# Performance work log

Hardware: AMD Instinct MI355X
Metric: run time of the kernel (lower is better)

The kernel has to match this reference:

```python
import jax, jax.numpy as jnp
import numpy as np

N = 100000
E = 1600000
BN_EPS = 1e-5


def setup_inputs() -> dict:
    key = jax.random.key(0)
    ks = jax.random.split(key, 32)
    rn = lambda k, shape, s=0.05: jax.random.normal(k, shape, jnp.float32) * s
    inp = {
        "x": jax.random.normal(ks[0], (N, 2), jnp.float32),
        "edge_index": jax.random.randint(ks[1], (2, E), 0, N, dtype=jnp.int64),
        # GIN conv1 mlp: Linear(1,256) -> BN(256) -> ReLU -> Linear(256,128)
        "w1": rn(ks[2], (1, 256)), "b1": rn(ks[3], (256,)),
        "g1": jax.random.uniform(ks[4], (256,), jnp.float32, 0.5, 1.5),
        "be1": rn(ks[5], (256,)),
        "m1": rn(ks[6], (256,)),
        "v1": jax.random.uniform(ks[7], (256,), jnp.float32, 0.5, 1.5),
        "w2": rn(ks[8], (256, 128)), "b2": rn(ks[9], (128,)),
        # GIN conv2 mlp: Linear(128,64) -> BN(64) -> ReLU -> Linear(64,64)
        "w3": rn(ks[10], (128, 64)), "b3": rn(ks[11], (64,)),
        "g2": jax.random.uniform(ks[12], (64,), jnp.float32, 0.5, 1.5),
        "be2": rn(ks[13], (64,)),
        "m2": rn(ks[14], (64,)),
        "v2": jax.random.uniform(ks[15], (64,), jnp.float32, 0.5, 1.5),
        # Bilinear(64, 64, 96)
        "wb": rn(ks[16], (96, 64, 64)), "bb": rn(ks[17], (96,)),
        # linear3: 96 -> 6
        "w5": rn(ks[18], (96, 6)), "b5": rn(ks[19], (6,)),
        # linear2: 6 -> 6
        "w6": rn(ks[20], (6, 6)), "b6": rn(ks[21], (6,)),
    }
    return inp


def reference(x, edge_index, w1, b1, g1, be1, m1, v1, w2, b2,
              w3, b3, g2, be2, m2, v2, w4_unused=None, wb=None, bb=None,
              w5=None, b5=None, w6=None, b6=None):
    # note: kept signature explicit below; see _reference
    raise NotImplementedError


def _bn(h, g, b, m, v):
    # inference-mode batchnorm with running stats
    return (h - m) * jax.lax.rsqrt(v + BN_EPS) * g + b


def reference(x, edge_index, w1, b1, g1, be1, m1, v1, w2, b2,
              w3, b3, g2, be2, m2, v2, wb, bb, w5, b5, w6, b6):
    src, dst = edge_index[0], edge_index[1]
    n = x.shape[0]

    def agg(h):
        # GIN sum aggregation: (1+eps)*x + sum_{j in N(i)} x_j, eps=0
        return h + jax.ops.segment_sum(h[src], dst, num_segments=n)

    def block(col):  # col: [n, 1]
        h = agg(col)
        h = jnp.maximum(_bn(h @ w1 + b1, g1, be1, m1, v1), 0.0) @ w2 + b2  # [n,128]
        h = agg(h)
        h = jnp.maximum(_bn(h @ w3 + b3, g2, be2, m2, v2), 0.0)            # mlp2 ends with BN+ReLU? no:
        return h

    # mlp2 = Linear(128,64)->BN(64)->ReLU->Linear(64,64); rebuild correctly inline:
    def block2(col):
        h = agg(col)
        h = jnp.maximum(_bn(h @ w1 + b1, g1, be1, m1, v1), 0.0) @ w2 + b2  # [n,128]
        h = agg(h)
        h = jnp.maximum(_bn(h @ w3 + b3, g2, be2, m2, v2), 0.0)
        return h

    h1 = block2(x[:, 1:2])  # column tmp-1 = 1 first
    h2 = block2(x[:, 0:1])  # then column 0
    # mlp2's final Linear(64,64) is folded below? No -- apply final linear of mlp2:
    # (handled in block2 already via w3 only; second linear uses separate weights)
    hb = jnp.einsum('ni,kij,nj->nk', h1, wb, h2) + bb  # Bilinear(64,64,96)
    h = jnp.maximum(hb @ w5 + b5, 0.0)                 # relu(linear3)
    h = h @ w6 + b6                                    # linear2
    return jax.nn.log_softmax(h, axis=1)
```

## Files before the change

kernel.cpp:

```cpp
#include <hip/hip_runtime.h>
#include <hip/hip_bf16.h>

#define NN 100000
#define NE 1600000
#define EPS 1e-5f
#define NCHUNK 98
#define NB 196
#define BCAP2 10240
#define RND 8192
#define NRND 196

typedef __attribute__((ext_vector_type(8))) short short8;
typedef __attribute__((ext_vector_type(4))) float f32x4;

__device__ __forceinline__ float b2f_lo(unsigned u){ return __uint_as_float(u << 16); }
__device__ __forceinline__ float b2f_hi(unsigned u){ return __uint_as_float(u & 0xffff0000u); }
__device__ __forceinline__ float b2f_u(unsigned short u){ return __uint_as_float(((unsigned)u) << 16); }
__device__ __forceinline__ unsigned short f2b(float f){
  __hip_bfloat16 h = __float2bfloat16(f);
  return __builtin_bit_cast(unsigned short, h);
}

__global__ void k_probe(const int* __restrict__ ei32, int* __restrict__ flag, int* __restrict__ gcur){
  __shared__ int cnt;
  if (threadIdx.x == 0) cnt = 0;
  __syncthreads();
  if (ei32[threadIdx.x * 2 + 1] == 0) atomicAdd(&cnt, 1);
  __syncthreads();
  if (threadIdx.x == 0) flag[0] = (cnt > 200) ? 1 : 0;
  for (int i = threadIdx.x; i < NB; i += 256) gcur[i] = i * BCAP2;
}

__global__ __launch_bounds__(1024) void k_bin(const void* __restrict__ ei, const int* __restrict__ flag,
                                              int* __restrict__ gcur, int* __restrict__ staged){
  __shared__ int hcnt[256];
  __shared__ int pref[256];
  __shared__ int bnd[200];
  __shared__ int hrun[196];
  __shared__ int gb[196];
  __shared__ int sbuf[RND];
  int t = threadIdx.x;
  int base = blockIdx.x * RND;
  bool f64 = (flag[0] != 0);
  int pay[8], bkt[8];
  #pragma unroll
  for (int k = 0; k < 8; ++k){
    int e = base + k * 1024 + t;
    if (e < NE){
      int src, dst;
      if (f64){ src = (int)((const long long*)ei)[e]; dst = (int)((const long long*)ei)[NE + e]; }
      else    { src = ((const int*)ei)[e];            dst = ((const int*)ei)[NE + e]; }
      pay[k] = (src << 9) | (dst & 511);
      bkt[k] = dst >> 9;
    } else { pay[k] = 0; bkt[k] = -1; }
  }
  if (t < 256) hcnt[t] = 0;
  __syncthreads();
  #pragma unroll
  for (int k = 0; k < 8; ++k)
    if (bkt[k] >= 0) atomicAdd(&hcnt[bkt[k]], 1);
  __syncthreads();
  if (t < 256) pref[t] = hcnt[t];
  __syncthreads();
  for (int off = 1; off < 256; off <<= 1){
    int v = 0;
    if (t < 256 && t >= off) v = pref[t - off];
    __syncthreads();
    if (t < 256) pref[t] += v;
    __syncthreads();
  }
  if (t < 196){
    int excl = pref[t] - hcnt[t];
    bnd[t] = excl;
    hrun[t] = excl;
    gb[t] = (hcnt[t] > 0) ? atomicAdd(&gcur[t], hcnt[t]) : 0;
  }
  if (t == 196) bnd[196] = 0;
  __syncthreads();
  if (t == 0) bnd[196] = pref[255];
  __syncthreads();
  #pragma unroll
  for (int k = 0; k < 8; ++k)
    if (bkt[k] >= 0){
      int lp = atomicAdd(&hrun[bkt[k]], 1);
      sbuf[lp] = pay[k];
    }
  __syncthreads();
  int total = bnd[196];
  for (int i = t; i < total; i += 1024){
    int b = 0;
    #pragma unroll
    for (int sh = 128; sh > 0; sh >>= 1)
      if (b + sh <= 196 && bnd[b + sh] <= i) b += sh;
    staged[gb[b] + (i - bnd[b])] = sbuf[i];
  }
}

__global__ __launch_bounds__(256) void k_bdeg(const int* __restrict__ staged, const int* __restrict__ gcur,
                                              int* __restrict__ deg){
  __shared__ int dcnt[512];
  int b = blockIdx.x, t = threadIdx.x;
  for (int l = t; l < 512; l += 256) dcnt[l] = 0;
  __syncthreads();
  int cnt = min(gcur[b] - b * BCAP2, BCAP2);
  const int* sp = staged + b * BCAP2;
  for (int i = t; i < cnt; i += 256)
    atomicAdd(&dcnt[sp[i] & 511], 1);
  __syncthreads();
  for (int l = t; l < 512; l += 256){
    int n = b * 512 + l;
    if (n < NN) deg[n] = dcnt[l];
  }
}

__global__ void k_scan1(const int* __restrict__ deg, int* __restrict__ cinc, int* __restrict__ part){
  __shared__ int b[1024];
  int i = blockIdx.x * 1024 + threadIdx.x;
  int v = (i < NN) ? deg[i] : 0;
  b[threadIdx.x] = v; __syncthreads();
  for (int off = 1; off < 1024; off <<= 1){
    int t = (threadIdx.x >= off) ? b[threadIdx.x - off] : 0;
    __syncthreads();
    b[threadIdx.x] += t;
    __syncthreads();
  }
  if (i < NN) cinc[i] = b[threadIdx.x];
  if (threadIdx.x == 1023) part[blockIdx.x] = b[1023];
}

__global__ void k_scan2(int* __restrict__ part, int nchunk){
  __shared__ int b[128];
  int tid = threadIdx.x;
  int v = (tid < nchunk) ? part[tid] : 0;
  b[tid] = v; __syncthreads();
  for (int off = 1; off < 128; off <<= 1){
    int t = (tid >= off) ? b[tid - off] : 0;
    __syncthreads();
    b[tid] += t;
    __syncthreads();
  }
  if (tid < nchunk) part[tid] = b[tid] - v;
}

__global__ void k_scan3(const int* __restrict__ deg, const int* __restrict__ cinc,
                        const int* __restrict__ part, int* __restrict__ rowp){
  int i = blockIdx.x * 1024 + threadIdx.x;
  if (i < NN){
    rowp[i] = cinc[i] - deg[i] + part[blockIdx.x];
  }
  if (i == 0) rowp[NN] = NE;
}

__global__ __launch_bounds__(256) void k_scatter2(const int* __restrict__ staged, const int* __restrict__ gcur,
                                                  const int* __restrict__ rowp, int* __restrict__ colidx){
  __shared__ int cur[512];
  int b = blockIdx.x, t = threadIdx.x;
  for (int l = t; l < 512; l += 256){
    int n = b * 512 + l;
    cur[l] = (n < NN) ? rowp[n] : 0;
  }
  __syncthreads();
  int cnt = min(gcur[b] - b * BCAP2, BCAP2);
  const int* sp = staged + b * BCAP2;
  for (int i = t; i < cnt; i += 256){
    int p = sp[i];
    int pos = atomicAdd(&cur[p & 511], 1);
    colidx[pos] = p >> 9;
  }
}

__global__ void k_prep_sort(const float* __restrict__ w1, const float* __restrict__ b1,
                            const float* __restrict__ g1, const float* __restrict__ be1,
                            const float* __restrict__ m1, const float* __restrict__ v1,
                            const float* __restrict__ w3, const float* __restrict__ b3,
                            const float* __restrict__ g2, const float* __restrict__ be2,
                            const float* __restrict__ m2, const float* __restrict__ v2,
                            float* __restrict__ aC, float* __restrict__ cC,
                            float* __restrict__ thrS, int* __restrict__ pos,
                            unsigned short* __restrict__ w3s, float* __restrict__ b3p){
  __shared__ float key[256];
  __shared__ int idx[256];
  int tid = threadIdx.x;
  {
    float inv = rsqrtf(v1[tid] + EPS);
    float sc = g1[tid] * inv;
    float a = w1[tid] * sc;
    float c = (b1[tid] - m1[tid]) * sc + be1[tid];
    aC[tid] = a; cC[tid] = c;
    key[tid] = (a != 0.0f) ? (-c / a) : __int_as_float(0x7f800000);
    idx[tid] = tid;
  }
  __syncthreads();
  for (int k = 2; k <= 256; k <<= 1){
    for (int j = k >> 1; j > 0; j >>= 1){
      int ixj = tid ^ j;
      if (ixj > tid){
        float k1 = key[tid], k2 = key[ixj];
        bool asc = ((tid & k) == 0);
        if ((k1 > k2) == asc){
          int i1 = idx[tid];
          key[tid] = k2; key[ixj] = k1;
          idx[tid] = idx[ixj]; idx[ixj] = i1;
        }
      }
      __syncthreads();
    }
  }
  thrS[tid] = key[tid];
  pos[idx[tid]] = tid;
  if (tid < 64){
    float i2 = rsqrtf(v2[tid] + EPS);
    b3p[tid] = (b3[tid] - m2[tid]) * i2 * g2[tid] + be2[tid];
  }
  for (int id = tid; id < 8192; id += 256){
    int cs = id >> 11, r = id & 2047;
    int kt = r >> 9;  r &= 511;
    int l = r >> 3;   int mi = r & 7;
    int krow = kt * 32 + (l >> 4) * 8 + mi;
    int col  = cs * 16 + (l & 15);
    float i2 = rsqrtf(v2[col] + EPS);
    w3s[id] = f2b(w3[krow * 64 + col] * i2 * g2[col]);
  }
}

__global__ void k_tab(const float* __restrict__ aC, const float* __restrict__ cC,
                      const int* __restrict__ pos, const float* __restrict__ w2,
                      const float* __restrict__ b2, unsigned short* __restrict__ tabG){
  __shared__ float ca[256], cc[256];
  int t = blockIdx.x;
  int tid = threadIdx.x;
  {
    float a = aC[tid], c = cC[tid];
    int p = pos[tid];
    bool act = (a > 0.f) ? (p < t) : ((a < 0.f) ? (p >= t) : (c > 0.f));
    ca[tid] = act ? a : 0.f;
    cc[tid] = act ? c : 0.f;
  }
  __syncthreads();
  int f = tid & 127, sel = tid >> 7;
  const float* coef = sel ? cc : ca;
  float acc = sel ? b2[f] : 0.f;
  #pragma unroll 8
  for (int j = 0; j < 256; ++j)
    acc = fmaf(coef[j], w2[j * 128 + f], acc);
  tabG[t * 256 + sel * 128 + f] = f2b(acc);
}

__global__ void k_wbS(const float* __restrict__ wb, unsigned short* __restrict__ wbS){
  int id = blockIdx.x * 256 + threadIdx.x;
  if (id >= 64 * 6144) return;
  int j = id / 6144;
  int r = id % 6144;
  int f = r >> 9;  r &= 511;
  int l = r >> 3;  int mi = r & 7;
  int kt = f / 6, cs = f % 6;
  int i = kt * 32 + (l >> 4) * 8 + mi;
  int k = cs * 16 + (l & 15);
  wbS[id] = f2b(wb[(k * 64 + i) * 64 + j]);
}

__global__ void k_sagg(const float* __restrict__ x, const int* __restrict__ rowp,
                       const int* __restrict__ colidx, const float* __restrict__ thrS,
                       float4* __restrict__ info){
  __shared__ float thr[256];
  thr[threadIdx.x] = thrS[threadIdx.x];
  __syncthreads();
  int n = blockIdx.x * 256 + threadIdx.x;
  if (n >= NN) return;
  float2 xv = ((const float2*)x)[n];
  float sA = xv.y, sB = xv.x;
  int s0 = rowp[n], s1 = rowp[n + 1];
  for (int e = s0; e < s1; ++e){
    int j = colidx[e];
    float2 xj = ((const float2*)x)[j];
    sA += xj.y; sB += xj.x;
  }
  int tA = 0, tB = 0;
  #pragma unroll
  for (int sh = 128; sh > 0; sh >>= 1){
    if (tA + sh <= 256 && thr[tA + sh - 1] < sA) tA += sh;
    if (tB + sh <= 256 && thr[tB + sh - 1] < sB) tB += sh;
  }
  info[n] = make_float4(sA, sB, __uint_as_float((unsigned)tA | ((unsigned)tB << 16)), 0.f);
}

__global__ __launch_bounds__(1024) void k_agg(
    const float4* __restrict__ info, const int* __restrict__ rowp,
    const int* __restrict__ colidx, const unsigned short* __restrict__ tabG,
    unsigned short* __restrict__ mA, unsigned short* __restrict__ mB){
  extern __shared__ unsigned tab32[];
  for (int i = threadIdx.x; i < 257 * 128; i += 1024)
    tab32[i] = ((const unsigned*)tabG)[i];
  __syncthreads();
  int lane = threadIdx.x & 63;
  int wv = (blockIdx.x * 1024 + threadIdx.x) >> 6;
  int nw = (gridDim.x * 1024) >> 6;
  int p  = lane >> 5;
  int fq = lane & 31;
  for (int n = wv; n < NN; n += nw){
    int s0 = rowp[n], cnt = rowp[n + 1] - s0 + 1;
    float a0 = 0.f, a1 = 0.f, a2 = 0.f, a3 = 0.f;
    for (int base = 0; base < cnt; base += 64){
      int nb = base + lane;
      float4 inf;
      if (nb < cnt){
        int j = (nb == 0) ? n : colidx[s0 + nb - 1];
        inf = info[j];
      } else inf = make_float4(0, 0, 0, 0);
      int m = min(cnt - base, 64);
      for (int q = 0; q < m; ++q){
        float sA = __shfl(inf.x, q);
        float sB = __shfl(inf.y, q);
        unsigned tt = __float_as_uint(__shfl(inf.z, q));
        float s = p ? sB : sA;
        int   t = p ? (int)(tt >> 16) : (int)(tt & 0xffffu);
        const unsigned* rp = &tab32[t * 128];
        uint2 av = *(const uint2*)&rp[fq * 2];
        uint2 bv = *(const uint2*)&rp[64 + fq * 2];
        a0 += fmaf(s, b2f_lo(av.x), b2f_lo(bv.x));
        a1 += fmaf(s, b2f_hi(av.x), b2f_hi(bv.x));
        a2 += fmaf(s, b2f_lo(av.y), b2f_lo(bv.y));
        a3 += fmaf(s, b2f_hi(av.y), b2f_hi(bv.y));
      }
    }
    unsigned short* dst = (p ? mB : mA) + n * 128 + fq * 4;
    unsigned o0 = (unsigned)f2b(a0) | ((unsigned)f2b(a1) << 16);
    unsigned o1 = (unsigned)f2b(a2) | ((unsigned)f2b(a3) << 16);
    *((uint2*)dst) = make_uint2(o0, o1);
  }
}

__global__ void k_mlp2(const unsigned short* __restrict__ mA, const unsigned short* __restrict__ mB,
                       const unsigned short* __restrict__ w3s, const float* __restrict__ b3p,
                       unsigned short* __restrict__ h1, unsigned short* __restrict__ h2T){
  int lane = threadIdx.x & 63;
  int tile = (blockIdx.x * blockDim.x + threadIdx.x) >> 6;
  const int NT = 2 * NN / 16;
  if (tile >= NT) return;
  bool pB = (tile >= NN / 16);
  const unsigned short* src = pB ? (mB + (size_t)(tile - NN / 16) * 16 * 128)
                                 : (mA + (size_t)tile * 16 * 128);
  short8 afr[4];
  {
    int row = lane & 15, ko = (lane >> 4) * 8;
    #pragma unroll
    for (int kt = 0; kt < 4; ++kt)
      afr[kt] = *(const short8*)(src + row * 128 + kt * 32 + ko);
  }
  f32x4 acc[4];
  #pragma unroll
  for (int cs = 0; cs < 4; ++cs){
    f32x4 a = {0.f, 0.f, 0.f, 0.f};
    #pragma unroll
    for (int kt = 0; kt < 4; ++kt){
      short8 b = *(const short8*)(w3s + ((cs * 4 + kt) * 64 + lane) * 8);
      a = __builtin_amdgcn_mfma_f32_16x16x32_bf16(afr[kt], b, a, 0, 0, 0);
    }
    acc[cs] = a;
  }
  int col0 = lane & 15, r0 = (lane >> 4) * 4;
  if (!pB){
    int nb = tile * 16;
    #pragma unroll
    for (int cs = 0; cs < 4; ++cs){
      float bias = b3p[cs * 16 + col0];
      #pragma unroll
      for (int r = 0; r < 4; ++r){
        float v = fmaxf(acc[cs][r] + bias, 0.f);
        h1[(size_t)(nb + r0 + r) * 64 + cs * 16 + col0] = f2b(v);
      }
    }
  } else {
    int nb = (tile - NN / 16) * 16;
    #pragma unroll
    for (int cs = 0; cs < 4; ++cs){
      float bias = b3p[cs * 16 + col0];
      unsigned p0 = (unsigned)f2b(fmaxf(acc[cs][0] + bias, 0.f)) | ((unsigned)f2b(fmaxf(acc[cs][1] + bias, 0.f)) << 16);
      unsigned p1 = (unsigned)f2b(fmaxf(acc[cs][2] + bias, 0.f)) | ((unsigned)f2b(fmaxf(acc[cs][3] + bias, 0.f)) << 16);
      *(uint2*)(h2T + (size_t)(cs * 16 + col0) * NN + nb + r0) = make_uint2(p0, p1);
    }
  }
}

__global__ __launch_bounds__(64, 2) void k_bil(
    const unsigned short* __restrict__ h1, const unsigned short* __restrict__ h2T,
    const unsigned short* __restrict__ wbS, const float* __restrict__ bbv,
    const float* __restrict__ w5, const float* __restrict__ b5,
    const float* __restrict__ w6, const float* __restrict__ b6,
    float* __restrict__ out){
  __shared__ unsigned short smem[64 * 98];
  int lane = threadIdx.x;
  int nb = blockIdx.x * 64;
  int rl = lane & 15, ko = (lane >> 4) * 8;
  {
    #pragma unroll 4
    for (int t = 0; t < 64; ++t){
      int i = t * 64 + lane;
      int j = i >> 6, l = (i >> 2) & 15, rt = i & 3;
      int n = nb + rt * 16 + l;
      smem[i] = (n < NN) ? h2T[(size_t)j * NN + n] : (unsigned short)0;
    }
  }
  float af[4][2][8];
  #pragma unroll
  for (int rt = 0; rt < 4; ++rt){
    int row = nb + rt * 16 + rl;
    #pragma unroll
    for (int kt = 0; kt < 2; ++kt){
      if (row < NN){
        uint4 rv = *(const uint4*)(h1 + (size_t)row * 64 + kt * 32 + ko);
        af[rt][kt][0] = b2f_lo(rv.x); af[rt][kt][1] = b2f_hi(rv.x);
        af[rt][kt][2] = b2f_lo(rv.y); af[rt][kt][3] = b2f_hi(rv.y);
        af[rt][kt][4] = b2f_lo(rv.z); af[rt][kt][5] = b2f_hi(rv.z);
        af[rt][kt][6] = b2f_lo(rv.w); af[rt][kt][7] = b2f_hi(rv.w);
      } else {
        #pragma unroll
        for (int e = 0; e < 8; ++e) af[rt][kt][e] = 0.f;
      }
    }
  }
  __syncthreads();
  f32x4 acc[4][6];
  #pragma unroll
  for (int rt = 0; rt < 4; ++rt)
    #pragma unroll
    for (int cs = 0; cs < 6; ++cs)
      acc[rt][cs] = (f32x4){0.f, 0.f, 0.f, 0.f};
  const unsigned short* wp = wbS + (size_t)lane * 8;
  for (int j = 0; j < 64; ++j){
    uint4 bf[2][6];
    #pragma unroll
    for (int kt = 0; kt < 2; ++kt)
      #pragma unroll
      for (int cs = 0; cs < 6; ++cs)
        bf[kt][cs] = *(const uint4*)(wp + (size_t)(j * 12 + kt * 6 + cs) * 512);
    uint2 hsv = *(const uint2*)(smem + j * 64 + rl * 4);
    #pragma unroll
    for (int rt = 0; rt < 4; ++rt){
      unsigned hw = (rt & 1) ? (rt & 2 ? hsv.y & 0xffff0000u : hsv.x & 0xffff0000u)
                             : (rt & 2 ? hsv.y << 16 : hsv.x << 16);
      float hs = __uint_as_float(hw);
      short8 a0, a1;
      #pragma unroll
      for (int e = 0; e < 8; ++e){
        a0[e] = (short)f2b(af[rt][0][e] * hs);
        a1[e] = (short)f2b(af[rt][1][e] * hs);
      }
      #pragma unroll
      for (int cs = 0; cs < 6; ++cs){
        acc[rt][cs] = __builtin_amdgcn_mfma_f32_16x16x32_bf16(a0, __builtin_bit_cast(short8, bf[0][cs]), acc[rt][cs], 0, 0, 0);
        acc[rt][cs] = __builtin_amdgcn_mfma_f32_16x16x32_bf16(a1, __builtin_bit_cast(short8, bf[1][cs]), acc[rt][cs], 0, 0, 0);
      }
    }
  }
  __syncthreads();
  {
    #pragma unroll
    for (int rt = 0; rt < 4; ++rt)
      #pragma unroll
      for (int cs = 0; cs < 6; ++cs){
        int col = cs * 16 + rl;
        float bias = bbv[col];
        #pragma unroll
        for (int r = 0; r < 4; ++r){
          int rowl = rt * 16 + (lane >> 4) * 4 + r;
          smem[rowl * 98 + col] = f2b(acc[rt][cs][r] + bias);
        }
      }
  }
  __syncthreads();
  {
    int n = nb + lane;
    if (n < NN){
      float u[6];
      #pragma unroll
      for (int q = 0; q < 6; ++q) u[q] = b5[q];
      for (int jj = 0; jj < 96; ++jj){
        float hv = b2f_u(smem[lane * 98 + jj]);
        #pragma unroll
        for (int q = 0; q < 6; ++q) u[q] = fmaf(hv, w5[jj * 6 + q], u[q]);
      }
      #pragma unroll
      for (int q = 0; q < 6; ++q) u[q] = fmaxf(u[q], 0.f);
      float v[6];
      #pragma unroll
      for (int q = 0; q < 6; ++q){
        float a2 = b6[q];
        #pragma unroll
        for (int pp = 0; pp < 6; ++pp) a2 = fmaf(u[pp], w6[pp * 6 + q], a2);
        v[q] = a2;
      }
      float mx = v[0];
      #pragma unroll
      for (int q = 1; q < 6; ++q) mx = fmaxf(mx, v[q]);
      float se = 0.f;
      #pragma unroll
      for (int q = 0; q < 6; ++q) se += expf(v[q] - mx);
      float ls = logf(se);
      #pragma unroll
      for (int q = 0; q < 6; ++q) out[(size_t)n * 6 + q] = v[q] - mx - ls;
    }
  }
}

extern "C" void kernel_launch(void* const* d_in, const int* in_sizes, int n_in,
                              void* d_out, int out_size, void* d_ws, size_t ws_size,
                              hipStream_t stream){
  const float* x   = (const float*)d_in[0];
  const void*  ei  = d_in[1];
  const float* w1  = (const float*)d_in[2];
  const float* b1  = (const float*)d_in[3];
  const float* g1  = (const float*)d_in[4];
  const float* be1 = (const float*)d_in[5];
  const float* m1  = (const float*)d_in[6];
  const float* v1  = (const float*)d_in[7];
  const float* w2  = (const float*)d_in[8];
  const float* b2  = (const float*)d_in[9];
  const float* w3  = (const float*)d_in[10];
  const float* b3  = (const float*)d_in[11];
  const float* g2  = (const float*)d_in[12];
  const float* be2 = (const float*)d_in[13];
  const float* m2  = (const float*)d_in[14];
  const float* v2  = (const float*)d_in[15];
  const float* wb  = (const float*)d_in[16];
  const float* bb  = (const float*)d_in[17];
  const float* w5  = (const float*)d_in[18];
  const float* b5  = (const float*)d_in[19];
  const float* w6  = (const float*)d_in[20];
  const float* b6  = (const float*)d_in[21];
  float* out = (float*)d_out;

  char* ws = (char*)d_ws;
  size_t off = 0;
  auto alloc = [&](size_t bytes) -> void* {
    void* p = ws + off;
    off += (bytes + 255) & ~(size_t)255;
    return p;
  };
  int* deg      = (int*)alloc((size_t)NN * 4);
  int* rowp     = (int*)alloc((size_t)(NN + 1) * 4);
  int* cinc     = (int*)alloc((size_t)NN * 4);
  int* part     = (int*)alloc(1024 * 4);
  int* flag     = (int*)alloc(256);
  int* gcur     = (int*)alloc((size_t)NB * 4 + 256);
  int* colidx   = (int*)alloc((size_t)NE * 4);
  float4* info  = (float4*)alloc((size_t)NN * 16);
  unsigned short* tabG = (unsigned short*)alloc(257 * 256 * 2);
  float* thrS   = (float*)alloc(256 * 4);
  float* aC     = (float*)alloc(256 * 4);
  float* cC     = (float*)alloc(256 * 4);
  int* pos      = (int*)alloc(256 * 4);
  unsigned short* w3s  = (unsigned short*)alloc(8192 * 2);
  float* b3p    = (float*)alloc(64 * 4);
  unsigned short* wbS  = (unsigned short*)alloc((size_t)393216 * 2);
  unsigned short* mA   = (unsigned short*)alloc((size_t)NN * 128 * 2);
  unsigned short* mB   = (unsigned short*)alloc((size_t)NN * 128 * 2);
  unsigned short* h1   = (unsigned short*)alloc((size_t)NN * 64 * 2);
  unsigned short* h2T  = (unsigned short*)alloc((size_t)NN * 64 * 2);
  int* staged   = (int*)mA;

  k_probe<<<1, 256, 0, stream>>>((const int*)ei, flag, gcur);
  k_bin<<<NRND, 1024, 0, stream>>>(ei, flag, gcur, staged);
  k_bdeg<<<NB, 256, 0, stream>>>(staged, gcur, deg);
  k_scan1<<<NCHUNK, 1024, 0, stream>>>(deg, cinc, part);
  k_scan2<<<1, 128, 0, stream>>>(part, NCHUNK);
  k_scan3<<<NCHUNK, 1024, 0, stream>>>(deg, cinc, part, rowp);
  k_scatter2<<<NB, 256, 0, stream>>>(staged, gcur, rowp, colidx);
  k_prep_sort<<<1, 256, 0, stream>>>(w1, b1, g1, be1, m1, v1, w3, b3, g2, be2, m2, v2,
                                     aC, cC, thrS, pos, w3s, b3p);
  k_tab<<<257, 256, 0, stream>>>(aC, cC, pos, w2, b2, tabG);
  k_wbS<<<(64 * 6144 + 255) / 256, 256, 0, stream>>>(wb, wbS);
  k_sagg<<<(NN + 255) / 256, 256, 0, stream>>>(x, rowp, colidx, thrS, info);
  hipFuncSetAttribute((const void*)k_agg, hipFuncAttributeMaxDynamicSharedMemorySize, 257 * 128 * 4);
  k_agg<<<256, 1024, 257 * 128 * 4, stream>>>(info, rowp, colidx, tabG, mA, mB);
  k_mlp2<<<(2 * NN / 16 + 3) / 4, 256, 0, stream>>>(mA, mB, w3s, b3p, h1, h2T);
  k_bil<<<(NN + 63) / 64, 64, 0, stream>>>(h1, h2T, wbS, bb, w5, b5, w6, b6, out);
}
```

Before: 340.1 us.

## Split bilinear j-loop across two waves with LDS reduction and B double-buffering

The bilinear kernel now runs 128 threads per block. Each of the two waves handles half of the 64 j-slices for the same 64 nodes. Wave 1 writes its partial accumulators to shared memory, and wave 0 adds them before the bias, linear3, linear2 and log-softmax epilogue. The weight fragment loads are double-buffered so the next j's B tiles load while the MFMAs for the current j run. This aims to raise parallelism and hide global-load latency in the MFMA loop, at the cost of a 24KB fp32 reduction buffer in LDS, an extra sync, and an epilogue done by only one wave.

```diff
diff --git a/kernel.cpp b/kernel.cpp
--- a/kernel.cpp
+++ b/kernel.cpp
@@ -382,24 +382,54 @@
   }
 }
 
-__global__ __launch_bounds__(64, 2) void k_bil(
+__device__ __forceinline__ void loadB(const unsigned short* wp, int j, uint4 (&bf)[2][6]){
+  #pragma unroll
+  for (int kt = 0; kt < 2; ++kt)
+    #pragma unroll
+    for (int cs = 0; cs < 6; ++cs)
+      bf[kt][cs] = *(const uint4*)(wp + (size_t)(j * 12 + kt * 6 + cs) * 512);
+}
+
+__device__ __forceinline__ void doJ(const float (&af)[4][2][8], const unsigned short* h2sT,
+                                    int j, int rl, const uint4 (&bf)[2][6], f32x4 (&acc)[4][6]){
+  uint2 hsv = *(const uint2*)(h2sT + j * 64 + rl * 4);
+  float hsr[4];
+  hsr[0] = b2f_lo(hsv.x); hsr[1] = b2f_hi(hsv.x);
+  hsr[2] = b2f_lo(hsv.y); hsr[3] = b2f_hi(hsv.y);
+  #pragma unroll
+  for (int rt = 0; rt < 4; ++rt){
+    float hs = hsr[rt];
+    short8 a0, a1;
+    #pragma unroll
+    for (int e = 0; e < 8; ++e){
+      a0[e] = (short)f2b(af[rt][0][e] * hs);
+      a1[e] = (short)f2b(af[rt][1][e] * hs);
+    }
+    #pragma unroll
+    for (int cs = 0; cs < 6; ++cs){
+      acc[rt][cs] = __builtin_amdgcn_mfma_f32_16x16x32_bf16(a0, __builtin_bit_cast(short8, bf[0][cs]), acc[rt][cs], 0, 0, 0);
+      acc[rt][cs] = __builtin_amdgcn_mfma_f32_16x16x32_bf16(a1, __builtin_bit_cast(short8, bf[1][cs]), acc[rt][cs], 0, 0, 0);
+    }
+  }
+}
+
+__global__ __launch_bounds__(128, 2) void k_bil(
     const unsigned short* __restrict__ h1, const unsigned short* __restrict__ h2T,
     const unsigned short* __restrict__ wbS, const float* __restrict__ bbv,
     const float* __restrict__ w5, const float* __restrict__ b5,
     const float* __restrict__ w6, const float* __restrict__ b6,
     float* __restrict__ out){
-  __shared__ unsigned short smem[64 * 98];
-  int lane = threadIdx.x;
+  __shared__ unsigned short h2sT[64 * 64];
+  __shared__ float red[64 * 96];
+  int tid = threadIdx.x;
+  int lane = tid & 63;
+  int wv = tid >> 6;
   int nb = blockIdx.x * 64;
   int rl = lane & 15, ko = (lane >> 4) * 8;
-  {
-    #pragma unroll 4
-    for (int t = 0; t < 64; ++t){
-      int i = t * 64 + lane;
-      int j = i >> 6, l = (i >> 2) & 15, rt = i & 3;
-      int n = nb + rt * 16 + l;
-      smem[i] = (n < NN) ? h2T[(size_t)j * NN + n] : (unsigned short)0;
-    }
+  for (int i = tid; i < 64 * 64; i += 128){
+    int j = i >> 6, l = (i >> 2) & 15, rt = i & 3;
+    int n = nb + rt * 16 + l;
+    h2sT[i] = (n < NN) ? h2T[(size_t)j * NN + n] : (unsigned short)0;
   }
   float af[4][2][8];
   #pragma unroll
@@ -427,34 +457,42 @@
     for (int cs = 0; cs < 6; ++cs)
       acc[rt][cs] = (f32x4){0.f, 0.f, 0.f, 0.f};
   const unsigned short* wp = wbS + (size_t)lane * 8;
-  for (int j = 0; j < 64; ++j){
-    uint4 bf[2][6];
-    #pragma unroll
-    for (int kt = 0; kt < 2; ++kt)
-      #pragma unroll
-      for (int cs = 0; cs < 6; ++cs)
-        bf[kt][cs] = *(const uint4*)(wp + (size_t)(j * 12 + kt * 6 + cs) * 512);
-    uint2 hsv = *(const uint2*)(smem + j * 64 + rl * 4);
-    #pragma unroll
-    for (int rt = 0; rt < 4; ++rt){
-      unsigned hw = (rt & 1) ? (rt & 2 ? hsv.y & 0xffff0000u : hsv.x & 0xffff0000u)
-                             : (rt & 2 ? hsv.y << 16 : hsv.x << 16);
-      float hs = __uint_as_float(hw);
-      short8 a0, a1;
-      #pragma unroll
-      for (int e = 0; e < 8; ++e){
-        a0[e] = (short)f2b(af[rt][0][e] * hs);
-        a1[e] = (short)f2b(af[rt][1][e] * hs);
-      }
+  int j0 = wv * 32, j1 = j0 + 32;
+  uint4 bfA[2][6], bfB[2][6];
+  loadB(wp, j0, bfA);
+  for (int j = j0; j < j1; j += 2){
+    loadB(wp, j + 1, bfB);
+    doJ(af, h2sT, j, rl, bfA, acc);
+    if (j + 2 < j1) loadB(wp, j + 2, bfA);
+    doJ(af, h2sT, j + 1, rl, bfB, acc);
+  }
+  if (wv == 1){
+    #pragma unroll
+    for (int rt = 0; rt < 4; ++rt)
       #pragma unroll
       for (int cs = 0; cs < 6; ++cs){
-        acc[rt][cs] = __builtin_amdgcn_mfma_f32_16x16x32_bf16(a0, __builtin_bit_cast(short8, bf[0][cs]), acc[rt][cs], 0, 0, 0);
-        acc[rt][cs] = __builtin_amdgcn_mfma_f32_16x16x32_bf16(a1, __builtin_bit_cast(short8, bf[1][cs]), acc[rt][cs], 0, 0, 0);
-      }
-    }
-  }
-  __syncthreads();
-  {
+        int col = cs * 16 + rl;
+        #pragma unroll
+        for (int r = 0; r < 4; ++r){
+          int row = rt * 16 + (lane >> 4) * 4 + r;
+          red[row * 96 + col] = acc[rt][cs][r];
+        }
+      }
+  }
+  __syncthreads();
+  if (wv == 0){
+    #pragma unroll
+    for (int rt = 0; rt < 4; ++rt)
+      #pragma unroll
+      for (int cs = 0; cs < 6; ++cs){
+        int col = cs * 16 + rl;
+        #pragma unroll
+        for (int r = 0; r < 4; ++r){
+          int row = rt * 16 + (lane >> 4) * 4 + r;
+          acc[rt][cs][r] += red[row * 96 + col];
+        }
+      }
+    unsigned short* hbs = (unsigned short*)red;
     #pragma unroll
     for (int rt = 0; rt < 4; ++rt)
       #pragma unroll
@@ -464,19 +502,16 @@
         #pragma unroll
         for (int r = 0; r < 4; ++r){
           int rowl = rt * 16 + (lane >> 4) * 4 + r;
-          smem[rowl * 98 + col] = f2b(acc[rt][cs][r] + bias);
+          hbs[rowl * 98 + col] = f2b(acc[rt][cs][r] + bias);
         }
       }
-  }
-  __syncthreads();
-  {
     int n = nb + lane;
     if (n < NN){
       float u[6];
       #pragma unroll
       for (int q = 0; q < 6; ++q) u[q] = b5[q];
       for (int jj = 0; jj < 96; ++jj){
-        float hv = b2f_u(smem[lane * 98 + jj]);
+        float hv = b2f_u(hbs[lane * 98 + jj]);
         #pragma unroll
         for (int q = 0; q < 6; ++q) u[q] = fmaf(hv, w5[jj * 6 + q], u[q]);
       }
@@ -574,5 +609,5 @@
   hipFuncSetAttribute((const void*)k_agg, hipFuncAttributeMaxDynamicSharedMemorySize, 257 * 128 * 4);
   k_agg<<<256, 1024, 257 * 128 * 4, stream>>>(info, rowp, colidx, tabG, mA, mB);
   k_mlp2<<<(2 * NN / 16 + 3) / 4, 256, 0, stream>>>(mA, mB, w3s, b3p, h1, h2T);
-  k_bil<<<(NN + 63) / 64, 64, 0, stream>>>(h1, h2T, wbS, bb, w5, b5, w6, b6, out);
-}
+  k_bil<<<(NN + 63) / 64, 128, 0, stream>>>(h1, h2T, wbS, bb, w5, b5, w6, b6, out);
+}
```

Result: slower. 533.0 us (+56.8%).
